# Kernel tuning notes

Hardware: AMD Instinct MI355X
Metric: run time of the kernel (lower is better)

## Reference

```python
import jax, jax.numpy as jnp
import numpy as np

B, K, P = 16, 64, 256
D_MODEL, EXPAND = 512, 2
D_INNER = D_MODEL * EXPAND  # 1024
D_CONV, D_FF, E_LAYERS = 4, 16, 4
DT_RANK = 32  # ceil(512/16)
RANK = 4


def rmsnorm(x, w, eps=1e-5):
    return x * jax.lax.rsqrt(jnp.mean(x * x, axis=-1, keepdims=True) + eps) * w


def selective_scan(u, delta, A, Bm, Cm, Dp):
    # u,delta: [b,l,d]; A: [d,n]; Bm,Cm: [b,l,n]; Dp: [d]
    dA = jnp.exp(jnp.einsum('bld,dn->bldn', delta, A))
    dBu = jnp.einsum('bld,bln,bld->bldn', delta, Bm, u)
    x0 = jnp.zeros((u.shape[0], u.shape[2], A.shape[1]), u.dtype)

    def step(x, t):
        dA_t, dBu_t, c_t = t
        x = dA_t * x + dBu_t
        return x, jnp.einsum('bdn,bn->bd', x, c_t)

    _, ys = jax.lax.scan(step, x0, (dA.swapaxes(0, 1), dBu.swapaxes(0, 1), Cm.swapaxes(0, 1)))
    return ys.swapaxes(0, 1) + u * Dp


def mamba_block(h, in_w, cw, cb, xp_w, dt_w, dt_b, A_log, Dp, out_w):
    b, l, _ = h.shape
    xr = h @ in_w.T  # [b,l,2*d_inner]
    x, res = xr[..., :D_INNER], xr[..., D_INNER:]
    # causal depthwise conv1d (torch pads d_conv-1 both sides then trims to l)
    xc = jax.lax.conv_general_dilated(
        x.swapaxes(1, 2), cw, (1,), [(D_CONV - 1, 0)],
        feature_group_count=D_INNER, dimension_numbers=('NCH', 'OIH', 'NCH'))
    x = jax.nn.silu((xc + cb[:, None]).swapaxes(1, 2))
    A = -jnp.exp(A_log)
    x_dbl = x @ xp_w.T
    delta = jax.nn.softplus(x_dbl[..., :DT_RANK] @ dt_w.T + dt_b)
    Bm = x_dbl[..., DT_RANK:DT_RANK + D_FF]
    Cm = x_dbl[..., DT_RANK + D_FF:]
    y = selective_scan(x, delta, A, Bm, Cm, Dp)
    y = y * jax.nn.silu(res)
    return y @ out_w.T


def setup_inputs() -> dict:
    key = jax.random.key(0)
    ks = iter(jax.random.split(key, 32))
    rn = lambda s, sc=0.02: jax.random.normal(next(ks), s, jnp.float32) * sc
    A_init = jnp.log(jnp.tile(jnp.arange(1, D_FF + 1, dtype=jnp.float32)[None, None, :],
                              (E_LAYERS, D_INNER, 1)))
    return {
        'inputs': jax.random.normal(next(ks), (B, K, P), jnp.float32),
        'sp_lin1_w': rn((D_MODEL, P)), 'sp_lin1_b': jnp.zeros((D_MODEL,)),
        'sp_lin2_w': rn((D_MODEL, D_MODEL)), 'sp_lin2_b': jnp.zeros((D_MODEL,)),
        'sp_gate_w': rn((D_MODEL, P)), 'sp_gate_b': jnp.zeros((D_MODEL,)),
        'sp_norm_w': jnp.ones((D_MODEL,)),
        'in_proj_w': rn((E_LAYERS, 2 * D_INNER, D_MODEL)),
        'conv_w': rn((E_LAYERS, D_INNER, 1, D_CONV)),
        'conv_b': jnp.zeros((E_LAYERS, D_INNER)),
        'x_proj_w': rn((E_LAYERS, DT_RANK + 2 * D_FF, D_INNER)),
        'dt_proj_w': rn((E_LAYERS, D_INNER, DT_RANK)),
        'dt_proj_b': jnp.zeros((E_LAYERS, D_INNER)),
        'A_log': A_init,
        'D': jnp.ones((E_LAYERS, D_INNER)),
        'out_proj_w': rn((E_LAYERS, D_MODEL, D_INNER)),
        'blk_norm_w': jnp.ones((E_LAYERS, D_MODEL)),
        'post_norm_w': jnp.ones((D_MODEL,)),
        'proj_w': rn((2 * P * RANK, D_MODEL)),
    }


def reference(inputs, sp_lin1_w, sp_lin1_b, sp_lin2_w, sp_lin2_b, sp_gate_w, sp_gate_b,
              sp_norm_w, in_proj_w, conv_w, conv_b, x_proj_w, dt_proj_w, dt_proj_b,
              A_log, D, out_proj_w, blk_norm_w, post_norm_w, proj_w):
    # SpatialEncoder, shared across lags (pure last-dim linears -> apply to [B,K,P])
    h = jax.nn.gelu(inputs @ sp_lin1_w.T + sp_lin1_b, approximate=False)
    h = h @ sp_lin2_w.T + sp_lin2_b
    g = jax.nn.sigmoid(inputs @ sp_gate_w.T + sp_gate_b)
    h = rmsnorm(h * g, sp_norm_w)  # [B,K,d_model]
    for l in range(E_LAYERS):
        h = mamba_block(rmsnorm(h, blk_norm_w[l]), in_proj_w[l], conv_w[l], conv_b[l],
                        x_proj_w[l], dt_proj_w[l], dt_proj_b[l], A_log[l], D[l],
                        out_proj_w[l]) + h
    h = rmsnorm(h, post_norm_w)
    out = h @ proj_w.T  # [B,K,2*P*RANK]
    U = out[..., :P * RANK].reshape(B, K, P, RANK)
    V = out[..., P * RANK:].reshape(B, K, P, RANK)
    coeffs = jnp.einsum('bkpr,bkqr->bkpq', U, V)
    preds = jnp.einsum('bkpq,bkq->bp', coeffs, inputs)
    return preds, coeffs
```

## Files before the change

### kernel.cpp

```cpp
#include <hip/hip_runtime.h>
#include <hip/hip_bf16.h>
#include <math.h>

namespace {

constexpr int SEQ    = 64;
constexpr int DINNER = 1024;
constexpr int DFF    = 16;
constexpr int DTRANK = 32;

typedef __attribute__((ext_vector_type(8))) short short8;
typedef __attribute__((ext_vector_type(4))) float f32x4;
typedef __attribute__((address_space(3))) unsigned int lds_u32_t;
typedef __attribute__((address_space(1))) unsigned int glb_u32_t;

__device__ __forceinline__ float sigm(float x) { return 1.f / (1.f + __expf(-x)); }
__device__ __forceinline__ short f2b(float v) {
    __hip_bfloat16 h = __float2bfloat16(v);
    return *(short*)&h;
}
__device__ __forceinline__ float b2f(short s) {
    union { unsigned u; float f; } c; c.u = ((unsigned)(unsigned short)s) << 16; return c.f;
}
__device__ __forceinline__ float softp(float v) {
    return fmaxf(v, 0.f) + log1pf(__expf(-fabsf(v)));
}

__device__ __forceinline__ void gemm_core64(
    f32x4 (&acc)[2][2],
    const short* __restrict__ A, int lda,
    const short* __restrict__ W, int ldw,
    int Kd, short* As, short* Bs, int m0, int n0)
{
    constexpr int SZ = 64 * 32;
    const int tid = threadIdx.x, wave = tid >> 6, lane = tid & 63;
    const int wm = wave >> 1, wn = wave & 1;
    const int l15 = lane & 15, kg = lane >> 4;

    const int p = wave * 64 + lane;
    const short* srcA = A + (size_t)(m0 + (p >> 2)) * lda + (p & 3) * 8;
    const short* srcB = W + (size_t)(n0 + (p >> 2)) * ldw + (p & 3) * 8;
    const int ob = (wave * 64) * 8;

    const int nt = Kd >> 5;
    __builtin_amdgcn_global_load_lds((const glb_u32_t*)srcA, (lds_u32_t*)(As + ob), 16, 0, 0);
    __builtin_amdgcn_global_load_lds((const glb_u32_t*)srcB, (lds_u32_t*)(Bs + ob), 16, 0, 0);

    for (int t = 0; t < nt; t++) {
        __syncthreads();
        if (t + 1 < nt) {
            const int k0 = (t + 1) * 32;
            const int s = ((t + 1) & 1) * SZ;
            __builtin_amdgcn_global_load_lds((const glb_u32_t*)(srcA + k0), (lds_u32_t*)(As + s + ob), 16, 0, 0);
            __builtin_amdgcn_global_load_lds((const glb_u32_t*)(srcB + k0), (lds_u32_t*)(Bs + s + ob), 16, 0, 0);
        }
        const short* Ab = As + (t & 1) * SZ;
        const short* Bb = Bs + (t & 1) * SZ;
        short8 af[2], bfr[2];
#pragma unroll
        for (int mi = 0; mi < 2; mi++)
            af[mi] = *(const short8*)(Ab + (wm * 32 + mi * 16 + l15) * 32 + kg * 8);
#pragma unroll
        for (int ni = 0; ni < 2; ni++)
            bfr[ni] = *(const short8*)(Bb + (wn * 32 + ni * 16 + l15) * 32 + kg * 8);
#pragma unroll
        for (int mi = 0; mi < 2; mi++)
#pragma unroll
            for (int ni = 0; ni < 2; ni++)
                acc[mi][ni] = __builtin_amdgcn_mfma_f32_16x16x32_bf16(af[mi], bfr[ni], acc[mi][ni], 0, 0, 0);
    }
}

__global__ __launch_bounds__(256) void prep_k(
    const float* __restrict__ lin1_w, const float* __restrict__ gate_w,
    const float* __restrict__ lin2_w, const float* __restrict__ in_proj_w,
    const float* __restrict__ out_proj_w, const float* __restrict__ proj_w,
    const float* __restrict__ x_proj_w, const float* __restrict__ dt_proj_w,
    const float* __restrict__ inputs, const float* __restrict__ blk_norm_w,
    const float* __restrict__ post_norm_w,
    short* __restrict__ wlin1gb, short* __restrict__ wlin2b, short* __restrict__ winpb,
    short* __restrict__ woutpb, short* __restrict__ wprojb, short* __restrict__ wxpdb,
    short* __restrict__ inputsb, float* __restrict__ preds, float* __restrict__ ss)
{
    const int blk = blockIdx.x, tid = threadIdx.x;
    if (blk < 1024) {
        const int wave = tid >> 6, lane = tid & 63;
        const int nrow = blk * 4 + wave;
        const int l = nrow >> 10, n = nrow & 1023;
        const float* dtw = dt_proj_w + (size_t)l * 32768 + n * 32;
        const float* xpw = x_proj_w + (size_t)l * 65536;
        float4 acc[4] = {};
        for (int r = 0; r < 32; r++) {
            const float s = dtw[r];
#pragma unroll
            for (int rep = 0; rep < 4; rep++) {
                const float4 xv = *(const float4*)(xpw + r * 1024 + rep * 256 + lane * 4);
                acc[rep].x = fmaf(s, xv.x, acc[rep].x);
                acc[rep].y = fmaf(s, xv.y, acc[rep].y);
                acc[rep].z = fmaf(s, xv.z, acc[rep].z);
                acc[rep].w = fmaf(s, xv.w, acc[rep].w);
            }
        }
        short* dst = wxpdb + (size_t)l * 1114112 + (size_t)(64 + n) * 1024;
#pragma unroll
        for (int rep = 0; rep < 4; rep++) {
            union { short sh[4]; uint2 u; } pk;
            pk.sh[0] = f2b(acc[rep].x); pk.sh[1] = f2b(acc[rep].y);
            pk.sh[2] = f2b(acc[rep].z); pk.sh[3] = f2b(acc[rep].w);
            *(uint2*)(dst + rep * 256 + lane * 4) = pk.u;
        }
    } else if (blk < 1088) {
#pragma unroll
        for (int rep = 0; rep < 4; rep++) {
            const int e = (blk - 1024) * 4096 + rep * 1024 + tid * 4;
            const int l = e >> 16, rowk = e & 65535;
            const float4 v = *(const float4*)(x_proj_w + (size_t)l * 65536 + rowk);
            union { short sh[4]; uint2 u; } pk;
            pk.sh[0] = f2b(v.x); pk.sh[1] = f2b(v.y); pk.sh[2] = f2b(v.z); pk.sh[3] = f2b(v.w);
            *(uint2*)(wxpdb + (size_t)l * 1114112 + rowk) = pk.u;
        }
    } else if (blk < 2048) {
        constexpr int pre[8] = {0, 128, 256, 512, 4608, 6656, 7680, 7936};
        for (int vb = blk - 1088; vb < 7936; vb += 960) {
            int s = 0;
#pragma unroll
            for (int i = 1; i < 7; i++) s += (vb >= pre[i]);
            const int e = (vb - pre[s]) * 1024 + tid * 4;
            const float* src; short* dst;
            bool hasG = false; const float* gp = nullptr;
            if      (s == 0) { src = lin1_w + e;     dst = wlin1gb + e; }
            else if (s == 1) { src = gate_w + e;     dst = wlin1gb + 131072 + e; }
            else if (s == 2) { src = lin2_w + e;     dst = wlin2b + e; }
            else if (s == 3) { src = in_proj_w + e;  dst = winpb + e;
                               hasG = true; gp = blk_norm_w + (e >> 20) * 512 + (e & 511); }
            else if (s == 4) { src = out_proj_w + e; dst = woutpb + e; }
            else if (s == 5) { src = proj_w + e;     dst = wprojb + e;
                               hasG = true; gp = post_norm_w + (e & 511); }
            else             { src = inputs + e;     dst = inputsb + e; }
            float4 v = *(const float4*)src;
            if (hasG) {
                const float4 gv = *(const float4*)gp;
                v.x *= gv.x; v.y *= gv.y; v.z *= gv.z; v.w *= gv.w;
            }
            union { short sh[4]; uint2 u; } pk;
            pk.sh[0] = f2b(v.x); pk.sh[1] = f2b(v.y); pk.sh[2] = f2b(v.z); pk.sh[3] = f2b(v.w);
            *(uint2*)dst = pk.u;
        }
    } else {
        const int i = (blk - 2048) * 256 + tid;
        if (i < 4096) preds[i] = 0.f;
        else ss[1024 + (i - 4096)] = 0.f;
    }
}

__global__ __launch_bounds__(256) void lin1gate_k(
    const short* __restrict__ A, const short* __restrict__ W,
    const float* __restrict__ b1, const float* __restrict__ b2,
    short* __restrict__ h1b, float* __restrict__ g)
{
    __shared__ short As[2 * 64 * 32];
    __shared__ short Bs[2 * 64 * 32];
    f32x4 acc[2][2] = {};
    const int m0 = blockIdx.y * 64, n0 = blockIdx.x * 64;
    gemm_core64(acc, A, 256, W, 256, 256, As, Bs, m0, n0);
    const int lane = threadIdx.x & 63, wave = threadIdx.x >> 6;
    const int wm = wave >> 1, wn = wave & 1, l15 = lane & 15, kg = lane >> 4;
#pragma unroll
    for (int ni = 0; ni < 2; ni++) {
        const int col = n0 + wn * 32 + ni * 16 + l15;
        const bool isG = col >= 512;
        const float b = isG ? b2[col - 512] : b1[col];
#pragma unroll
        for (int mi = 0; mi < 2; mi++)
#pragma unroll
            for (int j = 0; j < 4; j++) {
                const int row = m0 + wm * 32 + mi * 16 + kg * 4 + j;
                const float v = acc[mi][ni][j] + b;
                if (isG) g[(size_t)row * 512 + (col - 512)] = sigm(v);
                else     h1b[(size_t)row * 512 + col] = f2b(0.5f * v * (1.f + erff(v * 0.70710678f)));
            }
    }
}

__global__ __launch_bounds__(256) void lin2_k(
    const short* __restrict__ A, const short* __restrict__ W,
    const float* __restrict__ bias, const float* __restrict__ g, float* __restrict__ x)
{
    __shared__ short As[2 * 64 * 32];
    __shared__ short Bs[2 * 64 * 32];
    f32x4 acc[2][2] = {};
    const int m0 = blockIdx.y * 64, n0 = blockIdx.x * 64;
    gemm_core64(acc, A, 512, W, 512, 512, As, Bs, m0, n0);
    const int lane = threadIdx.x & 63, wave = threadIdx.x >> 6;
    const int wm = wave >> 1, wn = wave & 1, l15 = lane & 15, kg = lane >> 4;
#pragma unroll
    for (int ni = 0; ni < 2; ni++) {
        const int col = n0 + wn * 32 + ni * 16 + l15;
        const float b = bias[col];
#pragma unroll
        for (int mi = 0; mi < 2; mi++)
#pragma unroll
            for (int j = 0; j < 4; j++) {
                const int row = m0 + wm * 32 + mi * 16 + kg * 4 + j;
                x[(size_t)row * 512 + col] = (acc[mi][ni][j] + b) * g[(size_t)row * 512 + col];
            }
    }
}

__global__ __launch_bounds__(256) void rms_sp_k(
    const float* __restrict__ x, const float* __restrict__ w,
    float* __restrict__ h, short* __restrict__ hb, float* __restrict__ ss0)
{
    const int lane = threadIdx.x & 63;
    const int rowId = blockIdx.x * 4 + (threadIdx.x >> 6);
    const float* ip = x + (size_t)rowId * 512 + lane * 8;
    const float4 v1 = *(const float4*)ip;
    const float4 v2 = *(const float4*)(ip + 4);
    float sq = v1.x * v1.x + v1.y * v1.y + v1.z * v1.z + v1.w * v1.w
             + v2.x * v2.x + v2.y * v2.y + v2.z * v2.z + v2.w * v2.w;
#pragma unroll
    for (int off = 32; off > 0; off >>= 1) sq += __shfl_xor(sq, off, 64);
    const float rs = rsqrtf(sq * (1.f / 512.f) + 1e-5f);
    const float4 w1 = *(const float4*)(w + lane * 8);
    const float4 w2 = *(const float4*)(w + lane * 8 + 4);
    const float o[8] = { v1.x * rs * w1.x, v1.y * rs * w1.y, v1.z * rs * w1.z, v1.w * rs * w1.w,
                         v2.x * rs * w2.x, v2.y * rs * w2.y, v2.z * rs * w2.z, v2.w * rs * w2.w };
    float* op = h + (size_t)rowId * 512 + lane * 8;
    *(float4*)op       = make_float4(o[0], o[1], o[2], o[3]);
    *(float4*)(op + 4) = make_float4(o[4], o[5], o[6], o[7]);
    short8 pk;
#pragma unroll
    for (int i = 0; i < 8; i++) pk[i] = f2b(o[i]);
    *(short8*)(hb + (size_t)rowId * 512 + lane * 8) = pk;
    float s2 = 0.f;
#pragma unroll
    for (int i = 0; i < 8; i++) s2 = fmaf(o[i], o[i], s2);
#pragma unroll
    for (int off = 32; off > 0; off >>= 1) s2 += __shfl_xor(s2, off, 64);
    if (lane == 0) ss0[rowId] = s2;
}

union ConvU {
    struct { short As[2 * 64 * 32]; short Bs[2 * 64 * 32]; } gm;
    float cbuf[67][68];
};

__global__ __launch_bounds__(256) void inprojconv_k(
    const short* __restrict__ A, const short* __restrict__ W,
    const float* __restrict__ ss_in, const float* __restrict__ cw,
    const float* __restrict__ cb, short* __restrict__ xcb, short* __restrict__ srb)
{
    __shared__ ConvU u;
    f32x4 acc[2][2] = {};
    const int m0 = blockIdx.y * 64, n0 = blockIdx.x * 64;
    gemm_core64(acc, A, 512, W, 512, 512, u.gm.As, u.gm.Bs, m0, n0);
    const int tid = threadIdx.x;
    const int lane = tid & 63, wave = tid >> 6;
    const int wm = wave >> 1, wn = wave & 1, l15 = lane & 15, kg = lane >> 4;

#pragma unroll
    for (int mi = 0; mi < 2; mi++)
#pragma unroll
        for (int j = 0; j < 4; j++) {
            const int row = m0 + wm * 32 + mi * 16 + kg * 4 + j;
            const float r = rsqrtf(ss_in[row] * (1.f / 512.f) + 1e-5f);
#pragma unroll
            for (int ni = 0; ni < 2; ni++) acc[mi][ni][j] *= r;
        }

    if (n0 < 1024) {
        const int ccol = tid & 63;
        const int rg = tid >> 6;
        const int d = n0 + ccol;
        const float4 w4 = *(const float4*)(cw + d * 4);
        const float bia = cb[d];

        __syncthreads();
#pragma unroll
        for (int mi = 0; mi < 2; mi++)
#pragma unroll
            for (int ni = 0; ni < 2; ni++)
#pragma unroll
                for (int j = 0; j < 4; j++)
                    u.cbuf[3 + wm * 32 + mi * 16 + kg * 4 + j][wn * 32 + ni * 16 + l15] = acc[mi][ni][j];
        for (int i = tid; i < 3 * 68; i += 256) u.cbuf[i / 68][i % 68] = 0.f;
        __syncthreads();
#pragma unroll 4
        for (int k = 0; k < 16; k++) {
            const int row = rg + 4 * k;
            float v = bia + w4.x * u.cbuf[row][ccol] + w4.y * u.cbuf[row + 1][ccol]
                          + w4.z * u.cbuf[row + 2][ccol] + w4.w * u.cbuf[row + 3][ccol];
            v = v * sigm(v);
            xcb[(size_t)(m0 + row) * 1024 + d] = f2b(v);
        }
    } else {
#pragma unroll
        for (int ni = 0; ni < 2; ni++) {
            const int scol = n0 - 1024 + wn * 32 + ni * 16 + l15;
#pragma unroll
            for (int mi = 0; mi < 2; mi++)
#pragma unroll
                for (int j = 0; j < 4; j++) {
                    const int row = m0 + wm * 32 + mi * 16 + kg * 4 + j;
                    const float v = acc[mi][ni][j];
                    srb[(size_t)row * 1024 + scol] = f2b(v * sigm(v));
                }
        }
    }
}

union XsU {
    struct { short As[2 * 64 * 32]; short Bs[2 * 64 * 32]; } gm;
    struct { float dlt[64][68]; float BC[64][32]; } sc;
};

__global__ __launch_bounds__(256) void xpdscan_k(
    const short* __restrict__ A , const short* __restrict__ W ,
    const float* __restrict__ dtb, const float* __restrict__ Alog,
    const float* __restrict__ Dp, const short* __restrict__ srb, short* __restrict__ yb)
{
    __shared__ XsU u;
    const int dg = blockIdx.x, b = blockIdx.y;
    const int m0 = b * 64;
    const int tid = threadIdx.x;
    const int lane = tid & 63, wave = tid >> 6;
    const int wm = wave >> 1, wn = wave & 1, l15 = lane & 15, kg = lane >> 4;

    f32x4 accd[2][2] = {};
    gemm_core64(accd, A, 1024, W, 1024, 1024, u.gm.As, u.gm.Bs, m0, 64 + dg * 64);
    f32x4 accx[2][2] = {};
    gemm_core64(accx, A, 1024, W, 1024, 1024, u.gm.As, u.gm.Bs, m0, 0);

    __syncthreads();
#pragma unroll
    for (int ni = 0; ni < 2; ni++) {
        const int dl = wn * 32 + ni * 16 + l15;
        const float bb = dtb[dg * 64 + dl];
#pragma unroll
        for (int mi = 0; mi < 2; mi++)
#pragma unroll
            for (int j = 0; j < 4; j++)
                u.sc.dlt[wm * 32 + mi * 16 + kg * 4 + j][dl] = softp(accd[mi][ni][j] + bb);
    }
    if (wn == 1) {
#pragma unroll
        for (int ni = 0; ni < 2; ni++) {
            const int c = ni * 16 + l15;
#pragma unroll
            for (int mi = 0; mi < 2; mi++)
#pragma unroll
                for (int j = 0; j < 4; j++)
                    u.sc.BC[wm * 32 + mi * 16 + kg * 4 + j][c] = accx[mi][ni][j];
        }
    }
    __syncthreads();

    if (tid < 64) {
        const int d = dg * 64 + tid;
        float a[16], s[16];
#pragma unroll
        for (int n = 0; n < 16; n++) { a[n] = -__expf(Alog[(size_t)d * 16 + n]); s[n] = 0.f; }
        const float dv = Dp[d];
        const size_t base = (size_t)b * SEQ;
        float uu = b2f(A[base * DINNER + d]);
        float rr = b2f(srb[base * 1024 + d]);
        for (int l = 0; l < SEQ; l++) {
            float uu_n = 0.f, rr_n = 0.f;
            if (l + 1 < SEQ) {
                uu_n = b2f(A[(base + l + 1) * DINNER + d]);
                rr_n = b2f(srb[(base + l + 1) * 1024 + d]);
            }
            const float dlt = u.sc.dlt[l][tid];
            const float dbu = dlt * uu;
            float acc = 0.f;
#pragma unroll
            for (int n = 0; n < 16; n++) {
                s[n] = __expf(dlt * a[n]) * s[n] + dbu * u.sc.BC[l][n];
                acc = fmaf(s[n], u.sc.BC[l][16 + n], acc);
            }
            acc = fmaf(uu, dv, acc);
            yb[(base + l) * DINNER + d] = f2b(acc * rr);
            uu = uu_n; rr = rr_n;
        }
    }
}

__global__ __launch_bounds__(256) void outproj_k(
    const short* __restrict__ A, const short* __restrict__ W,
    float* __restrict__ h, short* __restrict__ hb, float* __restrict__ ss_out)
{
    __shared__ short As[2 * 64 * 32];
    __shared__ short Bs[2 * 64 * 32];
    f32x4 acc[2][2] = {};
    const int m0 = blockIdx.y * 64, n0 = blockIdx.x * 64;
    gemm_core64(acc, A, 1024, W, 1024, 1024, As, Bs, m0, n0);
    const int lane = threadIdx.x & 63, wave = threadIdx.x >> 6;
    const int wm = wave >> 1, wn = wave & 1, l15 = lane & 15, kg = lane >> 4;
    float vsq[2][4] = {};
#pragma unroll
    for (int ni = 0; ni < 2; ni++) {
        const int col = n0 + wn * 32 + ni * 16 + l15;
#pragma unroll
        for (int mi = 0; mi < 2; mi++)
#pragma unroll
            for (int j = 0; j < 4; j++) {
                const int row = m0 + wm * 32 + mi * 16 + kg * 4 + j;
                const float v = acc[mi][ni][j] + h[(size_t)row * 512 + col];
                h[(size_t)row * 512 + col] = v;
                hb[(size_t)row * 512 + col] = f2b(v);
                vsq[mi][j] = fmaf(v, v, vsq[mi][j]);
            }
    }
#pragma unroll
    for (int mi = 0; mi < 2; mi++)
#pragma unroll
        for (int j = 0; j < 4; j++) {
            float t = vsq[mi][j];
            t += __shfl_xor(t, 1, 64);
            t += __shfl_xor(t, 2, 64);
            t += __shfl_xor(t, 4, 64);
            t += __shfl_xor(t, 8, 64);
            if (l15 == 0) {
                const int row = m0 + wm * 32 + mi * 16 + kg * 4 + j;
                atomicAdd(ss_out + row, t);
            }
        }
}

__global__ __launch_bounds__(256) void projf_k(
    const short* __restrict__ A, const short* __restrict__ W,
    const float* __restrict__ ss_in, float* __restrict__ xr)
{
    __shared__ short As[2 * 64 * 32];
    __shared__ short Bs[2 * 64 * 32];
    f32x4 acc[2][2] = {};
    const int m0 = blockIdx.y * 64, n0 = blockIdx.x * 64;
    gemm_core64(acc, A, 512, W, 512, 512, As, Bs, m0, n0);
    const int lane = threadIdx.x & 63, wave = threadIdx.x >> 6;
    const int wm = wave >> 1, wn = wave & 1, l15 = lane & 15, kg = lane >> 4;
#pragma unroll
    for (int mi = 0; mi < 2; mi++)
#pragma unroll
        for (int j = 0; j < 4; j++) {
            const int row = m0 + wm * 32 + mi * 16 + kg * 4 + j;
            const float r = rsqrtf(ss_in[row] * (1.f / 512.f) + 1e-5f);
#pragma unroll
            for (int ni = 0; ni < 2; ni++) {
                const int col = n0 + wn * 32 + ni * 16 + l15;
                xr[(size_t)row * 2048 + col] = acc[mi][ni][j] * r;
            }
        }
}

__global__ __launch_bounds__(256) void coeffs_k(
    const float* __restrict__ outp, const float* __restrict__ inp,
    float* __restrict__ coeffs, float* __restrict__ preds)
{
    const int m = blockIdx.x;
    const int b = m >> 6;
    const int tid = threadIdx.x, wave = tid >> 6, lane = tid & 63;
    __shared__ float4 Us[256], Vs[256];
    __shared__ float ins[256];
    __shared__ float4 tpart[4];
    Us[tid] = *(const float4*)(outp + (size_t)m * 2048 + tid * 4);
    Vs[tid] = *(const float4*)(outp + (size_t)m * 2048 + 1024 + tid * 4);
    ins[tid] = inp[(size_t)m * 256 + tid];
    __syncthreads();
    const float4 vq0 = Vs[lane * 4 + 0], vq1 = Vs[lane * 4 + 1];
    const float4 vq2 = Vs[lane * 4 + 2], vq3 = Vs[lane * 4 + 3];
    float* cbase = coeffs + (size_t)m * 65536 + lane * 4;
#pragma unroll 4
    for (int i = 0; i < 64; i++) {
        const int pp = (wave << 6) + i;
        const float4 up = Us[pp];
        float4 c;
        c.x = up.x * vq0.x + up.y * vq0.y + up.z * vq0.z + up.w * vq0.w;
        c.y = up.x * vq1.x + up.y * vq1.y + up.z * vq1.z + up.w * vq1.w;
        c.z = up.x * vq2.x + up.y * vq2.y + up.z * vq2.z + up.w * vq2.w;
        c.w = up.x * vq3.x + up.y * vq3.y + up.z * vq3.z + up.w * vq3.w;
        *(float4*)(cbase + (size_t)pp * 256) = c;
    }
    const float iv = ins[tid];
    const float4 vm = Vs[tid];
    float4 t = make_float4(vm.x * iv, vm.y * iv, vm.z * iv, vm.w * iv);
#pragma unroll
    for (int off = 32; off > 0; off >>= 1) {
        t.x += __shfl_xor(t.x, off, 64);
        t.y += __shfl_xor(t.y, off, 64);
        t.z += __shfl_xor(t.z, off, 64);
        t.w += __shfl_xor(t.w, off, 64);
    }
    if (lane == 0) tpart[wave] = t;
    __syncthreads();
    const float4 t0 = tpart[0], t1 = tpart[1], t2 = tpart[2], t3 = tpart[3];
    const float4 tt = make_float4(t0.x + t1.x + t2.x + t3.x, t0.y + t1.y + t2.y + t3.y,
                                  t0.z + t1.z + t2.z + t3.z, t0.w + t1.w + t2.w + t3.w);
    const float4 up = Us[tid];
    const float pv = up.x * tt.x + up.y * tt.y + up.z * tt.z + up.w * tt.w;
    atomicAdd(preds + (size_t)b * 256 + tid, pv);
}

}

extern "C" void kernel_launch(void* const* d_in, const int* in_sizes, int n_in,
                              void* d_out, int out_size, void* d_ws, size_t ws_size,
                              hipStream_t stream)
{
    const float* inputs     = (const float*)d_in[0];
    const float* lin1_w     = (const float*)d_in[1];
    const float* lin1_b     = (const float*)d_in[2];
    const float* lin2_w     = (const float*)d_in[3];
    const float* lin2_b     = (const float*)d_in[4];
    const float* gate_w     = (const float*)d_in[5];
    const float* gate_b     = (const float*)d_in[6];
    const float* sp_norm_w  = (const float*)d_in[7];
    const float* in_proj_w  = (const float*)d_in[8];
    const float* conv_w     = (const float*)d_in[9];
    const float* conv_b     = (const float*)d_in[10];
    const float* x_proj_w   = (const float*)d_in[11];
    const float* dt_proj_w  = (const float*)d_in[12];
    const float* dt_proj_b  = (const float*)d_in[13];
    const float* A_log      = (const float*)d_in[14];
    const float* Dvec       = (const float*)d_in[15];
    const float* out_proj_w = (const float*)d_in[16];
    const float* blk_norm_w = (const float*)d_in[17];
    const float* post_norm_w= (const float*)d_in[18];
    const float* proj_w     = (const float*)d_in[19];

    float* ws = (float*)d_ws;
    float* h     = ws;
    float* xr    = ws + 524288;
    float* x     = ws + 2621440;
    float* g     = ws + 3145728;
    float* ss    = ws + 3670016;
    short* bfb     = (short*)(ws + 3676160);
    short* inputsb = bfb;
    short* h1b     = bfb + 262144;
    short* hb      = bfb + 786432;
    short* xcb     = bfb + 1310720;
    short* yb      = bfb + 2359296;
    short* srb     = bfb + 3407872;
    short* wlin1gb = bfb + 4456448;
    short* wlin2b  = bfb + 4718592;
    short* winpb   = bfb + 4980736;
    short* woutpb  = bfb + 9175040;
    short* wprojb  = bfb + 11272192;
    short* wxpdb   = bfb + 12320768;
    float* preds  = (float*)d_out;
    float* coeffs = (float*)d_out + 4096;

    const dim3 blk(256);

    prep_k<<<dim3(2080), blk, 0, stream>>>(
        lin1_w, gate_w, lin2_w, in_proj_w, out_proj_w, proj_w, x_proj_w, dt_proj_w,
        inputs, blk_norm_w, post_norm_w,
        wlin1gb, wlin2b, winpb, woutpb, wprojb, wxpdb, inputsb, preds, ss);

    lin1gate_k<<<dim3(16, 16), blk, 0, stream>>>(inputsb, wlin1gb, lin1_b, gate_b, h1b, g);
    lin2_k<<<dim3(8, 16), blk, 0, stream>>>(h1b, wlin2b, lin2_b, g, x);
    rms_sp_k<<<dim3(256), blk, 0, stream>>>(x, sp_norm_w, h, hb, ss);

    for (int l = 0; l < 4; l++) {
        inprojconv_k<<<dim3(32, 16), blk, 0, stream>>>(
            hb, winpb + (size_t)l * 1048576, ss + l * 1024,
            conv_w + (size_t)l * 4096, conv_b + l * 1024, xcb, srb);
        xpdscan_k<<<dim3(16, 16), blk, 0, stream>>>(
            xcb, wxpdb + (size_t)l * 1114112, dt_proj_b + l * 1024,
            A_log + (size_t)l * 16384, Dvec + l * 1024, srb, yb);
        outproj_k<<<dim3(8, 16), blk, 0, stream>>>(yb, woutpb + (size_t)l * 524288,
                                                   h, hb, ss + (l + 1) * 1024);
    }

    projf_k<<<dim3(32, 16), blk, 0, stream>>>(hb, wprojb, ss + 4096, xr);
    coeffs_k<<<dim3(1024), blk, 0, stream>>>(xr, inputs, coeffs, preds);
}
```

Baseline: 423.0 us.

## Trim x_proj fused weights, tile dt-fold through LDS, split outproj rows

The prep kernel now stages x_proj rows in shared memory and builds the folded dt weight with far fewer blocks. The fused x_proj/dt weight drops the unused dt-rank rows, so the stride goes from 1088 to 1056 rows. The scan kernel replaces its two GEMM passes with one fused K loop that computes delta and B/C together, so activation tiles are loaded once and the dead 32 columns are skipped. outproj uses 32-row tiles to double its grid for better occupancy, at the cost of loading the weight tile twice as often.

Result: slower. 545.6 us (+29.0%).

```diff
diff --git a/kernel.cpp b/kernel.cpp
--- a/kernel.cpp
+++ b/kernel.cpp
@@ -8,6 +8,7 @@
 constexpr int DINNER = 1024;
 constexpr int DFF    = 16;
 constexpr int DTRANK = 32;
+constexpr int WXPD_STRIDE = 1056 * 1024;
 
 typedef __attribute__((ext_vector_type(8))) short short8;
 typedef __attribute__((ext_vector_type(4))) float f32x4;
@@ -82,46 +83,51 @@
     short* __restrict__ woutpb, short* __restrict__ wprojb, short* __restrict__ wxpdb,
     short* __restrict__ inputsb, float* __restrict__ preds, float* __restrict__ ss)
 {
+    __shared__ float xs[32][256];
     const int blk = blockIdx.x, tid = threadIdx.x;
-    if (blk < 1024) {
+    if (blk < 256) {
+        const int l = blk >> 6;
+        const int r0 = (blk & 63) * 16;
         const int wave = tid >> 6, lane = tid & 63;
-        const int nrow = blk * 4 + wave;
-        const int l = nrow >> 10, n = nrow & 1023;
-        const float* dtw = dt_proj_w + (size_t)l * 32768 + n * 32;
         const float* xpw = x_proj_w + (size_t)l * 65536;
-        float4 acc[4] = {};
-        for (int r = 0; r < 32; r++) {
-            const float s = dtw[r];
-#pragma unroll
-            for (int rep = 0; rep < 4; rep++) {
-                const float4 xv = *(const float4*)(xpw + r * 1024 + rep * 256 + lane * 4);
-                acc[rep].x = fmaf(s, xv.x, acc[rep].x);
-                acc[rep].y = fmaf(s, xv.y, acc[rep].y);
-                acc[rep].z = fmaf(s, xv.z, acc[rep].z);
-                acc[rep].w = fmaf(s, xv.w, acc[rep].w);
-            }
-        }
-        short* dst = wxpdb + (size_t)l * 1114112 + (size_t)(64 + n) * 1024;
-#pragma unroll
         for (int rep = 0; rep < 4; rep++) {
-            union { short sh[4]; uint2 u; } pk;
-            pk.sh[0] = f2b(acc[rep].x); pk.sh[1] = f2b(acc[rep].y);
-            pk.sh[2] = f2b(acc[rep].z); pk.sh[3] = f2b(acc[rep].w);
-            *(uint2*)(dst + rep * 256 + lane * 4) = pk.u;
-        }
-    } else if (blk < 1088) {
+            for (int i = tid; i < 2048; i += 256) {
+                const int r = i >> 6, c = (i & 63) * 4;
+                *(float4*)&xs[r][c] = *(const float4*)(xpw + r * 1024 + rep * 256 + c);
+            }
+            __syncthreads();
+#pragma unroll
+            for (int rr = 0; rr < 4; rr++) {
+                const int row = r0 + wave * 4 + rr;
+                const float* dtw = dt_proj_w + (size_t)l * 32768 + row * 32;
+                float4 acc = make_float4(0.f, 0.f, 0.f, 0.f);
+                for (int r = 0; r < 32; r++) {
+                    const float s = dtw[r];
+                    const float4 xv = *(const float4*)&xs[r][lane * 4];
+                    acc.x = fmaf(s, xv.x, acc.x); acc.y = fmaf(s, xv.y, acc.y);
+                    acc.z = fmaf(s, xv.z, acc.z); acc.w = fmaf(s, xv.w, acc.w);
+                }
+                union { short sh[4]; uint2 u; } pk;
+                pk.sh[0] = f2b(acc.x); pk.sh[1] = f2b(acc.y);
+                pk.sh[2] = f2b(acc.z); pk.sh[3] = f2b(acc.w);
+                *(uint2*)(wxpdb + (size_t)l * WXPD_STRIDE + (size_t)(32 + row) * 1024
+                          + rep * 256 + lane * 4) = pk.u;
+            }
+            __syncthreads();
+        }
+    } else if (blk < 288) {
 #pragma unroll
         for (int rep = 0; rep < 4; rep++) {
-            const int e = (blk - 1024) * 4096 + rep * 1024 + tid * 4;
-            const int l = e >> 16, rowk = e & 65535;
-            const float4 v = *(const float4*)(x_proj_w + (size_t)l * 65536 + rowk);
+            const int idx = (blk - 256) * 4096 + rep * 1024 + tid * 4;
+            const int l = idx >> 15, off = idx & 32767;
+            const float4 v = *(const float4*)(x_proj_w + (size_t)l * 65536 + 32768 + off);
             union { short sh[4]; uint2 u; } pk;
             pk.sh[0] = f2b(v.x); pk.sh[1] = f2b(v.y); pk.sh[2] = f2b(v.z); pk.sh[3] = f2b(v.w);
-            *(uint2*)(wxpdb + (size_t)l * 1114112 + rowk) = pk.u;
-        }
-    } else if (blk < 2048) {
+            *(uint2*)(wxpdb + (size_t)l * WXPD_STRIDE + off) = pk.u;
+        }
+    } else if (blk < 1248) {
         constexpr int pre[8] = {0, 128, 256, 512, 4608, 6656, 7680, 7936};
-        for (int vb = blk - 1088; vb < 7936; vb += 960) {
+        for (int vb = blk - 288; vb < 7936; vb += 960) {
             int s = 0;
 #pragma unroll
             for (int i = 1; i < 7; i++) s += (vb >= pre[i]);
@@ -147,7 +153,7 @@
             *(uint2*)dst = pk.u;
         }
     } else {
-        const int i = (blk - 2048) * 256 + tid;
+        const int i = (blk - 1248) * 256 + tid;
         if (i < 4096) preds[i] = 0.f;
         else ss[1024 + (i - 4096)] = 0.f;
     }
@@ -310,7 +316,7 @@
 }
 
 union XsU {
-    struct { short As[2 * 64 * 32]; short Bs[2 * 64 * 32]; } gm;
+    struct { short As[2 * 64 * 32]; short Wd[2 * 64 * 32]; short BC[2 * 32 * 32]; } gm;
     struct { float dlt[64][68]; float BC[64][32]; } sc;
 };
 
@@ -326,10 +332,50 @@
     const int lane = tid & 63, wave = tid >> 6;
     const int wm = wave >> 1, wn = wave & 1, l15 = lane & 15, kg = lane >> 4;
 
+    constexpr int SZA = 64 * 32, SZBC = 32 * 32;
+    const int p = wave * 64 + lane;
+    const short* srcA  = A + (size_t)(m0 + (p >> 2)) * 1024 + (p & 3) * 8;
+    const short* srcWd = W + (size_t)(32 + dg * 64 + (p >> 2)) * 1024 + (p & 3) * 8;
+    const short* srcBC = W + (size_t)(p >> 2) * 1024 + (p & 3) * 8;
+    const int ob = (wave * 64) * 8;
+
     f32x4 accd[2][2] = {};
-    gemm_core64(accd, A, 1024, W, 1024, 1024, u.gm.As, u.gm.Bs, m0, 64 + dg * 64);
-    f32x4 accx[2][2] = {};
-    gemm_core64(accx, A, 1024, W, 1024, 1024, u.gm.As, u.gm.Bs, m0, 0);
+    f32x4 accx[2] = {};
+
+    __builtin_amdgcn_global_load_lds((const glb_u32_t*)srcA,  (lds_u32_t*)(u.gm.As + ob), 16, 0, 0);
+    __builtin_amdgcn_global_load_lds((const glb_u32_t*)srcWd, (lds_u32_t*)(u.gm.Wd + ob), 16, 0, 0);
+    if (wave < 2)
+        __builtin_amdgcn_global_load_lds((const glb_u32_t*)srcBC, (lds_u32_t*)(u.gm.BC + ob), 16, 0, 0);
+
+    for (int t = 0; t < 32; t++) {
+        __syncthreads();
+        if (t + 1 < 32) {
+            const int k0 = (t + 1) * 32;
+            const int sA = ((t + 1) & 1) * SZA, sBC = ((t + 1) & 1) * SZBC;
+            __builtin_amdgcn_global_load_lds((const glb_u32_t*)(srcA + k0),  (lds_u32_t*)(u.gm.As + sA + ob), 16, 0, 0);
+            __builtin_amdgcn_global_load_lds((const glb_u32_t*)(srcWd + k0), (lds_u32_t*)(u.gm.Wd + sA + ob), 16, 0, 0);
+            if (wave < 2)
+                __builtin_amdgcn_global_load_lds((const glb_u32_t*)(srcBC + k0), (lds_u32_t*)(u.gm.BC + sBC + ob), 16, 0, 0);
+        }
+        const short* Ab  = u.gm.As + (t & 1) * SZA;
+        const short* Wdb = u.gm.Wd + (t & 1) * SZA;
+        const short* BCb = u.gm.BC + (t & 1) * SZBC;
+        short8 af[2], wf[2], bcf;
+#pragma unroll
+        for (int mi = 0; mi < 2; mi++)
+            af[mi] = *(const short8*)(Ab + (wm * 32 + mi * 16 + l15) * 32 + kg * 8);
+#pragma unroll
+        for (int ni = 0; ni < 2; ni++)
+            wf[ni] = *(const short8*)(Wdb + (wn * 32 + ni * 16 + l15) * 32 + kg * 8);
+        bcf = *(const short8*)(BCb + (wn * 16 + l15) * 32 + kg * 8);
+#pragma unroll
+        for (int mi = 0; mi < 2; mi++) {
+#pragma unroll
+            for (int ni = 0; ni < 2; ni++)
+                accd[mi][ni] = __builtin_amdgcn_mfma_f32_16x16x32_bf16(af[mi], wf[ni], accd[mi][ni], 0, 0, 0);
+            accx[mi] = __builtin_amdgcn_mfma_f32_16x16x32_bf16(af[mi], bcf, accx[mi], 0, 0, 0);
+        }
+    }
 
     __syncthreads();
 #pragma unroll
@@ -342,16 +388,13 @@
             for (int j = 0; j < 4; j++)
                 u.sc.dlt[wm * 32 + mi * 16 + kg * 4 + j][dl] = softp(accd[mi][ni][j] + bb);
     }
-    if (wn == 1) {
-#pragma unroll
-        for (int ni = 0; ni < 2; ni++) {
-            const int c = ni * 16 + l15;
-#pragma unroll
-            for (int mi = 0; mi < 2; mi++)
-#pragma unroll
-                for (int j = 0; j < 4; j++)
-                    u.sc.BC[wm * 32 + mi * 16 + kg * 4 + j][c] = accx[mi][ni][j];
-        }
+    {
+        const int c = wn * 16 + l15;
+#pragma unroll
+        for (int mi = 0; mi < 2; mi++)
+#pragma unroll
+            for (int j = 0; j < 4; j++)
+                u.sc.BC[wm * 32 + mi * 16 + kg * 4 + j][c] = accx[mi][j];
     }
     __syncthreads();
 
@@ -389,28 +432,56 @@
     const short* __restrict__ A, const short* __restrict__ W,
     float* __restrict__ h, short* __restrict__ hb, float* __restrict__ ss_out)
 {
-    __shared__ short As[2 * 64 * 32];
+    __shared__ short As[2 * 32 * 32];
     __shared__ short Bs[2 * 64 * 32];
-    f32x4 acc[2][2] = {};
-    const int m0 = blockIdx.y * 64, n0 = blockIdx.x * 64;
-    gemm_core64(acc, A, 1024, W, 1024, 1024, As, Bs, m0, n0);
-    const int lane = threadIdx.x & 63, wave = threadIdx.x >> 6;
-    const int wm = wave >> 1, wn = wave & 1, l15 = lane & 15, kg = lane >> 4;
+    constexpr int SZA = 32 * 32, SZB = 64 * 32;
+    const int m0 = blockIdx.y * 32, n0 = blockIdx.x * 64;
+    const int tid = threadIdx.x, wave = tid >> 6, lane = tid & 63;
+    const int l15 = lane & 15, kg = lane >> 4;
+
+    const int p = wave * 64 + lane;
+    const short* srcA = A + (size_t)(m0 + (p >> 2)) * 1024 + (p & 3) * 8;
+    const short* srcB = W + (size_t)(n0 + (p >> 2)) * 1024 + (p & 3) * 8;
+    const int ob = (wave * 64) * 8;
+
+    f32x4 acc[2] = {};
+    if (wave < 2)
+        __builtin_amdgcn_global_load_lds((const glb_u32_t*)srcA, (lds_u32_t*)(As + ob), 16, 0, 0);
+    __builtin_amdgcn_global_load_lds((const glb_u32_t*)srcB, (lds_u32_t*)(Bs + ob), 16, 0, 0);
+
+    for (int t = 0; t < 32; t++) {
+        __syncthreads();
+        if (t + 1 < 32) {
+            const int k0 = (t + 1) * 32;
+            const int sA = ((t + 1) & 1) * SZA, sB = ((t + 1) & 1) * SZB;
+            if (wave < 2)
+                __builtin_amdgcn_global_load_lds((const glb_u32_t*)(srcA + k0), (lds_u32_t*)(As + sA + ob), 16, 0, 0);
+            __builtin_amdgcn_global_load_lds((const glb_u32_t*)(srcB + k0), (lds_u32_t*)(Bs + sB + ob), 16, 0, 0);
+        }
+        const short* Ab = As + (t & 1) * SZA;
+        const short* Bb = Bs + (t & 1) * SZB;
+        short8 af[2], bf;
+#pragma unroll
+        for (int mi = 0; mi < 2; mi++)
+            af[mi] = *(const short8*)(Ab + (mi * 16 + l15) * 32 + kg * 8);
+        bf = *(const short8*)(Bb + (wave * 16 + l15) * 32 + kg * 8);
+#pragma unroll
+        for (int mi = 0; mi < 2; mi++)
+            acc[mi] = __builtin_amdgcn_mfma_f32_16x16x32_bf16(af[mi], bf, acc[mi], 0, 0, 0);
+    }
+
+    const int col = n0 + wave * 16 + l15;
     float vsq[2][4] = {};
 #pragma unroll
-    for (int ni = 0; ni < 2; ni++) {
-        const int col = n0 + wn * 32 + ni * 16 + l15;
-#pragma unroll
-        for (int mi = 0; mi < 2; mi++)
-#pragma unroll
-            for (int j = 0; j < 4; j++) {
-                const int row = m0 + wm * 32 + mi * 16 + kg * 4 + j;
-                const float v = acc[mi][ni][j] + h[(size_t)row * 512 + col];
-                h[(size_t)row * 512 + col] = v;
-                hb[(size_t)row * 512 + col] = f2b(v);
-                vsq[mi][j] = fmaf(v, v, vsq[mi][j]);
-            }
-    }
+    for (int mi = 0; mi < 2; mi++)
+#pragma unroll
+        for (int j = 0; j < 4; j++) {
+            const int row = m0 + mi * 16 + kg * 4 + j;
+            const float v = acc[mi][j] + h[(size_t)row * 512 + col];
+            h[(size_t)row * 512 + col] = v;
+            hb[(size_t)row * 512 + col] = f2b(v);
+            vsq[mi][j] = v * v;
+        }
 #pragma unroll
     for (int mi = 0; mi < 2; mi++)
 #pragma unroll
@@ -421,7 +492,7 @@
             t += __shfl_xor(t, 4, 64);
             t += __shfl_xor(t, 8, 64);
             if (l15 == 0) {
-                const int row = m0 + wm * 32 + mi * 16 + kg * 4 + j;
+                const int row = m0 + mi * 16 + kg * 4 + j;
                 atomicAdd(ss_out + row, t);
             }
         }
@@ -551,7 +622,7 @@
 
     const dim3 blk(256);
 
-    prep_k<<<dim3(2080), blk, 0, stream>>>(
+    prep_k<<<dim3(1280), blk, 0, stream>>>(
         lin1_w, gate_w, lin2_w, in_proj_w, out_proj_w, proj_w, x_proj_w, dt_proj_w,
         inputs, blk_norm_w, post_norm_w,
         wlin1gb, wlin2b, winpb, woutpb, wprojb, wxpdb, inputsb, preds, ss);
@@ -565,9 +636,9 @@
             hb, winpb + (size_t)l * 1048576, ss + l * 1024,
             conv_w + (size_t)l * 4096, conv_b + l * 1024, xcb, srb);
         xpdscan_k<<<dim3(16, 16), blk, 0, stream>>>(
-            xcb, wxpdb + (size_t)l * 1114112, dt_proj_b + l * 1024,
+            xcb, wxpdb + (size_t)l * WXPD_STRIDE, dt_proj_b + l * 1024,
             A_log + (size_t)l * 16384, Dvec + l * 1024, srb, yb);
-        outproj_k<<<dim3(8, 16), blk, 0, stream>>>(yb, woutpb + (size_t)l * 524288,
+        outproj_k<<<dim3(8, 32), blk, 0, stream>>>(yb, woutpb + (size_t)l * 524288,
                                                    h, hb, ss + (l + 1) * 1024);
     }
 
```
